# Optimization experiments

Measured on AMD Instinct MI355X. Metric: run time of the kernel, lower is better.

## Reference

```python
import jax, jax.numpy as jnp
import numpy as np

NUM_OBJECTS = 6          # self.NUM_OBJECTS
SCORE_THRESH = 1e-4      # self.score_tresh
NMS_THRESHS = jnp.asarray(np.arange(0.001, 1.0, 0.1), dtype=jnp.float32)  # 10 thresholds
K_CAND = 1024            # fixed-shape cap on (proposal,class) candidates per image
CLASS_OFFSET = 4096.0    # > max image coord; batched_nms per-class offset trick


def _iou_matrix(b):
    # b: [K,4] xyxy -> [K,K] IoU
    x1, y1, x2, y2 = b[:, 0], b[:, 1], b[:, 2], b[:, 3]
    area = (x2 - x1) * (y2 - y1)
    iw = jnp.clip(jnp.minimum(x2[:, None], x2[None, :]) - jnp.maximum(x1[:, None], x1[None, :]), 0.0)
    ih = jnp.clip(jnp.minimum(y2[:, None], y2[None, :]) - jnp.maximum(y1[:, None], y1[None, :]), 0.0)
    inter = iw * ih
    union = area[:, None] + area[None, :] - inter
    return jnp.where(union > 0, inter / union, 0.0)


def _greedy_nms(iou, valid, thresh):
    # candidates are pre-sorted by descending score; sequential greedy suppression
    K = valid.shape[0]
    ar = jnp.arange(K)
    def body(i, keep):
        sup = keep[i] & (iou[i] > thresh) & (ar > i)
        return keep & ~sup
    return jax.lax.fori_loop(0, K, body, valid)


def _per_image(logits, boxes, feats, hw):
    # logits [N,81], boxes [N,80,4], feats [N,2048], hw [2] (h,w)
    C = boxes.shape[1]
    probs = jax.nn.softmax(logits, axis=-1)[:, :C]          # drop background class
    h = hw[0].astype(boxes.dtype)
    w = hw[1].astype(boxes.dtype)
    b = jnp.stack([jnp.clip(boxes[..., 0], 0.0, w),         # clip to image
                   jnp.clip(boxes[..., 1], 0.0, h),
                   jnp.clip(boxes[..., 2], 0.0, w),
                   jnp.clip(boxes[..., 3], 0.0, h)], axis=-1)
    scores = probs.reshape(-1)                              # [N*C]
    vals, idx = jax.lax.top_k(jnp.where(scores > SCORE_THRESH, scores, -1.0), K_CAND)
    cand_valid = vals > SCORE_THRESH
    cb = b.reshape(-1, 4)[idx]                              # [K,4]
    cls = (idx % C).astype(boxes.dtype)
    prop = idx // C                                         # proposal row index
    iou = _iou_matrix(cb + cls[:, None] * CLASS_OFFSET)     # per-class NMS via offsets
    keeps = jax.vmap(lambda t: _greedy_nms(iou, cand_valid, t))(NMS_THRESHS)  # [T,K]
    counts = keeps.sum(axis=1)
    # torch loop: break at first (smallest) thresh yielding len(ids)==6, i.e. >=6 kept
    ok = counts >= NUM_OBJECTS
    t_sel = jnp.where(jnp.any(ok), jnp.argmax(ok), NMS_THRESHS.shape[0] - 1)
    keep = keeps[t_sel]
    _, top = jax.lax.top_k(jnp.where(keep, vals, -jnp.inf), NUM_OBJECTS)
    ids = prop[top]                                         # [6]
    return feats[ids].T                                     # [2048, 6] (permute(1,0))


def _forward(cls_logits, boxes, feature_pooled, image_hw):
    return jax.vmap(_per_image)(cls_logits, boxes, feature_pooled, image_hw)  # [B,2048,6]


def setup_inputs() -> dict:
    key = jax.random.key(0)
    k1, k2, k3, k4, k5 = jax.random.split(key, 5)
    B, N, C, D = 8, 1000, 80, 2048
    cls_logits = jax.random.normal(k1, (B, N, C + 1), dtype=jnp.float32)
    ctr = jax.random.uniform(k2, (B, N, C, 2), minval=0.0, maxval=800.0)
    sz = jax.random.uniform(k3, (B, N, C, 2), minval=8.0, maxval=200.0)
    boxes = jnp.concatenate([ctr - sz * 0.5, ctr + sz * 0.5], axis=-1).astype(jnp.float32)
    feature_pooled = jax.random.normal(k4, (B, N, D), dtype=jnp.float32)
    image_hw = jax.random.randint(k5, (B, 2), 600, 800, dtype=jnp.int32)
    return {"cls_logits": cls_logits, "boxes": boxes,
            "feature_pooled": feature_pooled, "image_hw": image_hw}


def reference(cls_logits, boxes, feature_pooled, image_hw):
    return _forward(cls_logits, boxes, feature_pooled, image_hw)
```

## Files before the change

### kernel.cpp

```cpp
#include <hip/hip_runtime.h>
#include <cmath>
#include <cstdint>

#define NB 8
#define NPROP 1000
#define NCLS 80
#define NLOG 81
#define KCAND 1024
#define NTH 10
#define DFEAT 2048
#define NOBJ 6
#define NSCORE (NPROP*NCLS)
#define HBLK 8
#define HCHUNK (NSCORE/HBLK)
#define PCHUNK (NPROP/HBLK)
#define CCAP 64
#define GMAX 2048

constexpr size_t OFF_SCORES = 0;
constexpr size_t OFF_H1     = OFF_SCORES + (size_t)NB * NSCORE * 4;
constexpr size_t OFF_H2     = OFF_H1 + (size_t)NB * HBLK * 2048 * 4;
constexpr size_t OFF_PIV    = OFF_H2 + (size_t)NB * HBLK * 2048 * 4;
constexpr size_t OFF_CBUF   = OFF_PIV + (size_t)NB * 8 * 4;
constexpr size_t OFF_GCNT   = OFF_CBUF + (size_t)NB * GMAX * 8;
constexpr size_t OFF_S1P    = OFF_GCNT + (size_t)NB * 4096 * 4;
constexpr size_t OFF_S2P    = OFF_S1P + (size_t)NB * 2048 * 4;
constexpr size_t OFF_CX1    = OFF_S2P + (size_t)NB * 2048 * 4;
constexpr size_t SZ_CARR    = (size_t)NB * KCAND * 4;
constexpr size_t OFF_CY1    = OFF_CX1 + SZ_CARR;
constexpr size_t OFF_CX2    = OFF_CY1 + SZ_CARR;
constexpr size_t OFF_CY2    = OFF_CX2 + SZ_CARR;
constexpr size_t OFF_CAREA  = OFF_CY2 + SZ_CARR;
constexpr size_t OFF_CPROP  = OFF_CAREA + SZ_CARR;
constexpr size_t OFF_VALIDW = OFF_CPROP + SZ_CARR;
constexpr size_t OFF_CCNT   = OFF_VALIDW + (size_t)NB * 16 * 8;
constexpr size_t OFF_CLIST  = OFF_CCNT + (size_t)NB * NCLS * 4;
constexpr size_t OFF_KEEPS  = OFF_CLIST + (size_t)NB * NCLS * CCAP * 4;

__device__ __forceinline__ float nms_th(int t) {
    return (float)(0.001 + 0.1 * (double)t);
}

__device__ __forceinline__ unsigned score_vkey(float v) {
    float vv = (v > 1e-4f) ? v : -1.0f;
    unsigned bits = __float_as_uint(vv);
    unsigned u = (bits & 0x80000000u) ? ~bits : (bits | 0x80000000u);
    return ~u;
}

__device__ __forceinline__ void scan2048(unsigned a, unsigned b, unsigned* pre,
                                         unsigned K, int* out_b, int* out_rem) {
    __shared__ unsigned wsum[16];
    int tid = threadIdx.x;
    unsigned p = a + b;
    unsigned x = p;
    #pragma unroll
    for (int d = 1; d < 64; d <<= 1) {
        unsigned y = __shfl_up(x, (unsigned)d, 64);
        if ((tid & 63) >= d) x += y;
    }
    if ((tid & 63) == 63) wsum[tid >> 6] = x;
    __syncthreads();
    if (tid < 16) {
        unsigned w = wsum[tid];
        #pragma unroll
        for (int d = 1; d < 16; d <<= 1) {
            unsigned y = __shfl_up(w, (unsigned)d, 64);
            if (tid >= d) w += y;
        }
        wsum[tid] = w;
    }
    __syncthreads();
    unsigned wex = (tid >= 64) ? wsum[(tid >> 6) - 1] : 0u;
    unsigned E = x + wex - p;
    pre[2 * tid]     = E;
    pre[2 * tid + 1] = E + a;
    if (E < K && E + a >= K)              { *out_b = 2 * tid;     *out_rem = (int)(K - E); }
    else if (E + a < K && E + a + b >= K) { *out_b = 2 * tid + 1; *out_rem = (int)(K - (E + a)); }
}

__global__ __launch_bounds__(1024) void k_softhist(const float* __restrict__ logits,
                                                   float* __restrict__ scores,
                                                   unsigned* __restrict__ hist1) {
    __shared__ unsigned hh[2048];
    int img = blockIdx.x >> 3, blk = blockIdx.x & 7;
    int tid = threadIdx.x, wid = tid >> 6, lane = tid & 63;
    hh[tid] = 0; hh[tid + 1024] = 0;
    __syncthreads();
    for (int p = wid; p < PCHUNK; p += 16) {
        int prop = blk * PCHUNK + p;
        const float* L = logits + ((size_t)img * NPROP + prop) * NLOG;
        float l0 = L[lane];
        float l1 = (lane < 17) ? L[64 + lane] : -INFINITY;
        float m = fmaxf(l0, l1);
        #pragma unroll
        for (int o = 32; o > 0; o >>= 1) m = fmaxf(m, __shfl_xor(m, o, 64));
        float e0 = expf(l0 - m);
        float e1 = (lane < 17) ? expf(l1 - m) : 0.f;
        float s = e0 + e1;
        #pragma unroll
        for (int o = 32; o > 0; o >>= 1) s += __shfl_xor(s, o, 64);
        float* op = scores + ((size_t)img * NPROP + prop) * NCLS;
        float p0 = e0 / s;
        op[lane] = p0;
        atomicAdd(&hh[score_vkey(p0) >> 21], 1u);
        if (lane < 16) {
            float p1 = e1 / s;
            op[64 + lane] = p1;
            atomicAdd(&hh[score_vkey(p1) >> 21], 1u);
        }
    }
    __syncthreads();
    unsigned* outp = hist1 + ((size_t)img * HBLK + blk) * 2048;
    outp[tid] = hh[tid];
    outp[tid + 1024] = hh[tid + 1024];
}

__global__ __launch_bounds__(1024) void k_hist2p(const float* __restrict__ scores,
                                                 const unsigned* __restrict__ hist1,
                                                 unsigned* __restrict__ hist2,
                                                 int* __restrict__ piv,
                                                 unsigned* __restrict__ gcg) {
    __shared__ unsigned hh[2048];
    __shared__ int sb, sr;
    int img = blockIdx.x >> 3, blk = blockIdx.x & 7;
    int tid = threadIdx.x;
    if (tid < 512) gcg[img * 4096 + blk * 512 + tid] = 0;
    if (tid == 0) { sb = 0; sr = 1; }
    __syncthreads();
    {
        unsigned a1 = 0, b1v = 0;
        const unsigned* h1 = hist1 + (size_t)img * HBLK * 2048;
        #pragma unroll
        for (int s = 0; s < HBLK; ++s) {
            a1  += h1[s * 2048 + 2 * tid];
            b1v += h1[s * 2048 + 2 * tid + 1];
        }
        scan2048(a1, b1v, hh, KCAND, &sb, &sr);
    }
    __syncthreads();
    hh[tid] = 0; hh[tid + 1024] = 0;
    __syncthreads();
    unsigned b1 = (unsigned)sb & 2047u;
    const float4* sc4 = (const float4*)(scores + (size_t)img * NSCORE + (size_t)blk * HCHUNK);
    #define H2S(val) { unsigned vk = score_vkey(val); \
                       if ((vk >> 21) == b1) atomicAdd(&hh[(vk >> 10) & 2047u], 1u); }
    for (int e4 = tid; e4 < HCHUNK / 4; e4 += 1024) {
        float4 v = sc4[e4];
        H2S(v.x) H2S(v.y) H2S(v.z) H2S(v.w)
    }
    #undef H2S
    __syncthreads();
    unsigned* outp = hist2 + ((size_t)img * HBLK + blk) * 2048;
    outp[tid] = hh[tid];
    outp[tid + 1024] = hh[tid + 1024];
    if (blk == 0 && tid == 0) {
        piv[img * 8 + 0] = sb;
        piv[img * 8 + 1] = sr;
    }
}

__global__ __launch_bounds__(1024) void k_gatherp(const float* __restrict__ scores,
                                                  const unsigned* __restrict__ hist1,
                                                  const unsigned* __restrict__ hist2,
                                                  int* __restrict__ piv,
                                                  unsigned long long* __restrict__ cbuf,
                                                  unsigned* __restrict__ gcg,
                                                  unsigned* __restrict__ s1pg,
                                                  unsigned* __restrict__ s2pg,
                                                  int* __restrict__ ccnt,
                                                  unsigned long long* __restrict__ validw,
                                                  unsigned long long* __restrict__ keeps) {
    __shared__ unsigned s1p[2048];
    __shared__ unsigned s2p[2048];
    __shared__ int sb1, sr1, sb2, sr2;
    int img = blockIdx.x >> 3, blk = blockIdx.x & 7;
    int tid = threadIdx.x;
    if (blockIdx.x == 0) {
        if (tid < NB * NCLS) ccnt[tid] = 0;
        if (tid >= 640 && tid < 640 + NB * 16) validw[tid - 640] = 0ULL;
    }
    if (blockIdx.x == 1) {
        for (int k = tid; k < NB * NTH * 16; k += 1024) keeps[k] = 0ULL;
    }
    if (tid == 0) { sb1 = 0; sr1 = 1; sb2 = 0; sr2 = 1; }
    __syncthreads();
    {
        unsigned a1 = 0, b1v = 0;
        const unsigned* h1 = hist1 + (size_t)img * HBLK * 2048;
        #pragma unroll
        for (int s = 0; s < HBLK; ++s) {
            a1  += h1[s * 2048 + 2 * tid];
            b1v += h1[s * 2048 + 2 * tid + 1];
        }
        scan2048(a1, b1v, s1p, KCAND, &sb1, &sr1);
    }
    __syncthreads();
    {
        unsigned a2 = 0, b2v = 0;
        const unsigned* h2 = hist2 + (size_t)img * HBLK * 2048;
        #pragma unroll
        for (int s = 0; s < HBLK; ++s) {
            a2  += h2[s * 2048 + 2 * tid];
            b2v += h2[s * 2048 + 2 * tid + 1];
        }
        scan2048(a2, b2v, s2p, (unsigned)sr1, &sb2, &sr2);
    }
    __syncthreads();
    unsigned b1 = (unsigned)sb1 & 2047u;
    unsigned sb2m = (unsigned)sb2 & 2047u;
    unsigned T22 = (b1 << 11) | sb2m;
    const float4* sc4 = (const float4*)(scores + (size_t)img * NSCORE + (size_t)blk * HCHUNK);
    unsigned long long* cb = cbuf + (size_t)img * GMAX;
    unsigned* gc = gcg + img * 4096;
    #define GAS(val, ei) { unsigned vk = score_vkey(val); unsigned t22 = vk >> 10; \
        if (t22 <= T22) { \
            unsigned h = vk >> 21; unsigned g, base; \
            if (h == b1) { unsigned sub = t22 & 2047u; g = 2048u + sub; base = s1p[b1] + s2p[sub]; } \
            else         { g = h;                      base = s1p[h]; } \
            unsigned slot = atomicAdd(&gc[g], 1u); \
            unsigned posn = base + slot; \
            if (posn < GMAX) cb[posn] = ((unsigned long long)vk << 32) | (unsigned)(ei); } }
    for (int e4 = tid; e4 < HCHUNK / 4; e4 += 1024) {
        float4 v = sc4[e4];
        int e = blk * HCHUNK + 4 * e4;
        GAS(v.x, e) GAS(v.y, e + 1) GAS(v.z, e + 2) GAS(v.w, e + 3)
    }
    #undef GAS
    if (blk == 0) {
        s1pg[img * 2048 + tid] = s1p[tid];
        s1pg[img * 2048 + tid + 1024] = s1p[tid + 1024];
        s2pg[img * 2048 + tid] = s2p[tid];
        s2pg[img * 2048 + tid + 1024] = s2p[tid + 1024];
        if (tid == 0) piv[img * 8 + 4] = sb2;
    }
}

__global__ __launch_bounds__(256) void k_rankcand(const unsigned long long* __restrict__ cbuf,
                                                  const int* __restrict__ piv,
                                                  const unsigned* __restrict__ gcg,
                                                  const unsigned* __restrict__ s1pg,
                                                  const unsigned* __restrict__ s2pg,
                                                  const float* __restrict__ boxes,
                                                  const int* __restrict__ hw,
                                                  float* __restrict__ cx1, float* __restrict__ cy1,
                                                  float* __restrict__ cx2, float* __restrict__ cy2,
                                                  float* __restrict__ car, int* __restrict__ cprop,
                                                  unsigned long long* __restrict__ validw,
                                                  int* __restrict__ ccnt, int* __restrict__ clist) {
    int img = blockIdx.x >> 3, sl = blockIdx.x & 7;
    int tid = threadIdx.x;
    unsigned b1   = (unsigned)piv[img * 8 + 0] & 2047u;
    unsigned sb2m = (unsigned)piv[img * 8 + 4] & 2047u;
    const unsigned* s1p = s1pg + img * 2048;
    const unsigned* s2p = s2pg + img * 2048;
    const unsigned* gc  = gcg + img * 4096;
    const unsigned long long* cb = cbuf + (size_t)img * GMAX;
    int cnt = (int)(s1p[b1] + s2p[sb2m] + gc[2048u + sb2m]);
    if (cnt > GMAX || cnt < 0) cnt = GMAX;
    int p = sl * 256 + tid;
    if (p < cnt) {
        unsigned long long akey = cb[p];
        unsigned vk = (unsigned)(akey >> 32);
        unsigned h = vk >> 21;
        unsigned base, gsz;
        if (h == b1) {
            unsigned sub = (vk >> 10) & 2047u;
            base = s1p[b1] + s2p[sub];
            gsz  = gc[2048u + sub];
        } else {
            base = s1p[h];
            gsz  = gc[h];
        }
        unsigned r_ = base;
        unsigned qe = base + gsz;
        if (qe > (unsigned)GMAX) qe = (unsigned)GMAX;
        for (unsigned q = base; q < qe; ++q)
            r_ += (cb[q] < akey) ? 1u : 0u;
        int r = (int)r_;
        unsigned idx = (unsigned)akey;
        int prop = (int)(idx / NCLS);
        if (r >= 0 && r < KCAND && (unsigned)prop < NPROP) {
            unsigned u = ~vk;
            const unsigned uth = __float_as_uint(1e-4f) | 0x80000000u;
            bool valid = u > uth;
            int cls = (int)(idx - (unsigned)prop * NCLS);
            const float4 bx = *(const float4*)(boxes + ((((size_t)img * NPROP + prop) * NCLS + cls) << 2));
            float fh = (float)hw[img * 2 + 0];
            float fw = (float)hw[img * 2 + 1];
            float x1 = fminf(fmaxf(bx.x, 0.f), fw);
            float y1 = fminf(fmaxf(bx.y, 0.f), fh);
            float x2 = fminf(fmaxf(bx.z, 0.f), fw);
            float y2 = fminf(fmaxf(bx.w, 0.f), fh);
            float offc = __fmul_rn((float)cls, 4096.0f);
            x1 = __fadd_rn(x1, offc); y1 = __fadd_rn(y1, offc);
            x2 = __fadd_rn(x2, offc); y2 = __fadd_rn(y2, offc);
            float area = __fmul_rn(__fsub_rn(x2, x1), __fsub_rn(y2, y1));
            int o = img * KCAND + r;
            cx1[o] = x1; cy1[o] = y1; cx2[o] = x2; cy2[o] = y2;
            car[o] = area; cprop[o] = prop;
            if (valid) atomicOr(&validw[img * 16 + (r >> 6)], 1ULL << (r & 63));
            int slot = atomicAdd(&ccnt[img * NCLS + cls], 1);
            if (slot < CCAP) clist[(img * NCLS + cls) * CCAP + slot] = r;
        }
    }
}

__global__ __launch_bounds__(256) void k_cnms(const int* __restrict__ ccnt,
                                              const int* __restrict__ clist,
                                              const float* __restrict__ cx1,
                                              const float* __restrict__ cy1,
                                              const float* __restrict__ cx2,
                                              const float* __restrict__ cy2,
                                              const float* __restrict__ car,
                                              const unsigned long long* __restrict__ validw,
                                              unsigned long long* __restrict__ keeps) {
    int gid  = blockIdx.x * 4 + (threadIdx.x >> 6);
    int lane = threadIdx.x & 63;
    if (gid >= NB * NCLS) return;
    int img = gid / NCLS, cls = gid - img * NCLS;
    int n = ccnt[img * NCLS + cls];
    if (n > CCAP) n = CCAP;
    if (n == 0) return;
    int r = (lane < n) ? clist[(img * NCLS + cls) * CCAP + lane] : 0x7fffffff;
    int pos = 0;
    for (int j = 0; j < n; ++j) {
        int rj = __shfl(r, j, 64);
        pos += (rj < r) ? 1 : 0;
    }
    int srt = 0;
    for (int j = 0; j < n; ++j) {
        int pj = __shfl(pos, j, 64);
        int rj = __shfl(r, j, 64);
        if (pj == lane) srt = rj;
    }
    srt &= (KCAND - 1);
    bool act = lane < n;
    int base = img * KCAND;
    float x1 = 0, y1 = 0, x2 = 0, y2 = 0, ar = 0;
    bool val = false;
    if (act) {
        x1 = cx1[base + srt]; y1 = cy1[base + srt];
        x2 = cx2[base + srt]; y2 = cy2[base + srt]; ar = car[base + srt];
        val = (validw[img * 16 + (srt >> 6)] >> (srt & 63)) & 1ULL;
    }
    unsigned long long m[NTH];
    #pragma unroll
    for (int t = 0; t < NTH; ++t) m[t] = 0ULL;
    for (int b = 0; b < n; ++b) {
        float xj1 = __shfl(x1, b, 64), yj1 = __shfl(y1, b, 64);
        float xj2 = __shfl(x2, b, 64), yj2 = __shfl(y2, b, 64);
        float aj  = __shfl(ar, b, 64);
        float iw = fmaxf(__fsub_rn(fminf(x2, xj2), fmaxf(x1, xj1)), 0.f);
        float ih = fmaxf(__fsub_rn(fminf(y2, yj2), fmaxf(y1, yj1)), 0.f);
        float inter = __fmul_rn(iw, ih);
        float uni   = __fsub_rn(__fadd_rn(ar, aj), inter);
        float iou   = (uni > 0.f) ? __fdiv_rn(inter, uni) : 0.f;
        if (act && b < lane) {
            #pragma unroll
            for (int t = 0; t < NTH; ++t)
                if (iou > nms_th(t)) m[t] |= 1ULL << b;
        }
    }
    unsigned long long vmask = __ballot(act && val);
    for (int t = 0; t < NTH; ++t) {
        unsigned long long keep = vmask;
        for (int it = 0; it <= n; ++it) {
            bool nk = act && val && ((m[t] & keep) == 0ULL);
            unsigned long long nb = __ballot(nk);
            if (nb == keep) break;
            keep = nb;
        }
        if (act && ((keep >> lane) & 1ULL))
            atomicOr(&keeps[((size_t)img * NTH + t) * 16 + (srt >> 6)], 1ULL << (srt & 63));
    }
}

__global__ __launch_bounds__(256) void k_selfeat(const unsigned long long* __restrict__ keeps,
                                                 const int* __restrict__ cprop,
                                                 const float* __restrict__ feats,
                                                 float* __restrict__ outp) {
    __shared__ int scnt[NTH];
    __shared__ unsigned long long skw[16];
    __shared__ int stsel;
    __shared__ int sids[NOBJ];
    int img = blockIdx.x >> 3;
    int tid = threadIdx.x;
    if (tid < NTH) scnt[tid] = 0;
    __syncthreads();
    if (tid < NTH * 16) {
        unsigned long long w = keeps[(size_t)img * NTH * 16 + tid];
        int pc = __popcll(w);
        if (pc) atomicAdd(&scnt[tid >> 4], pc);
    }
    __syncthreads();
    if (tid == 0) {
        int tsel = NTH - 1;
        for (int t = 0; t < NTH; ++t) if (scnt[t] >= NOBJ) { tsel = t; break; }
        stsel = tsel;
    }
    __syncthreads();
    if (tid < 16) skw[tid] = keeps[((size_t)img * NTH + stsel) * 16 + tid];
    __syncthreads();
    if (tid == 0) {
        int got = 0;
        for (int k = 0; k < 16 && got < NOBJ; ++k) {
            unsigned long long x = skw[k];
            while (x && got < NOBJ) {
                int b = __builtin_ctzll(x);
                int sid = cprop[img * KCAND + k * 64 + b];
                sids[got++] = ((unsigned)sid < NPROP) ? sid : 0;
                x &= x - 1;
            }
        }
        for (int k = 0; k < 16 && got < NOBJ; ++k) {
            unsigned long long x = ~skw[k];
            while (x && got < NOBJ) {
                int b = __builtin_ctzll(x);
                int sid = cprop[img * KCAND + k * 64 + b];
                sids[got++] = ((unsigned)sid < NPROP) ? sid : 0;
                x &= x - 1;
            }
        }
    }
    __syncthreads();
    int d = (blockIdx.x & 7) * 256 + tid;
    const float* fb = feats + (size_t)img * NPROP * DFEAT;
    float* ob = outp + ((size_t)img * DFEAT + d) * NOBJ;
    #pragma unroll
    for (int s = 0; s < NOBJ; ++s)
        ob[s] = fb[(size_t)sids[s] * DFEAT + d];
}

extern "C" void kernel_launch(void* const* d_in, const int* in_sizes, int n_in,
                              void* d_out, int out_size, void* d_ws, size_t ws_size,
                              hipStream_t stream) {
    const float* logits = (const float*)d_in[0];
    const float* boxes  = (const float*)d_in[1];
    const float* feats  = (const float*)d_in[2];
    const int*   hw     = (const int*)d_in[3];
    float* outp = (float*)d_out;

    char* ws = (char*)d_ws;
    float*              scores = (float*)(ws + OFF_SCORES);
    unsigned*           hist1  = (unsigned*)(ws + OFF_H1);
    unsigned*           hist2  = (unsigned*)(ws + OFF_H2);
    int*                piv    = (int*)(ws + OFF_PIV);
    unsigned long long* cbuf   = (unsigned long long*)(ws + OFF_CBUF);
    unsigned*           gcg    = (unsigned*)(ws + OFF_GCNT);
    unsigned*           s1pg   = (unsigned*)(ws + OFF_S1P);
    unsigned*           s2pg   = (unsigned*)(ws + OFF_S2P);
    float* cx1 = (float*)(ws + OFF_CX1);
    float* cy1 = (float*)(ws + OFF_CY1);
    float* cx2 = (float*)(ws + OFF_CX2);
    float* cy2 = (float*)(ws + OFF_CY2);
    float* car = (float*)(ws + OFF_CAREA);
    int*   cprop = (int*)(ws + OFF_CPROP);
    unsigned long long* validw = (unsigned long long*)(ws + OFF_VALIDW);
    int*   ccnt  = (int*)(ws + OFF_CCNT);
    int*   clist = (int*)(ws + OFF_CLIST);
    unsigned long long* keeps  = (unsigned long long*)(ws + OFF_KEEPS);

    k_softhist<<<NB * HBLK, 1024, 0, stream>>>(logits, scores, hist1);
    k_hist2p<<<NB * HBLK, 1024, 0, stream>>>(scores, hist1, hist2, piv, gcg);
    k_gatherp<<<NB * HBLK, 1024, 0, stream>>>(scores, hist1, hist2, piv, cbuf,
                                              gcg, s1pg, s2pg, ccnt, validw, keeps);
    k_rankcand<<<NB * HBLK, 256, 0, stream>>>(cbuf, piv, gcg, s1pg, s2pg, boxes, hw,
                                              cx1, cy1, cx2, cy2, car, cprop,
                                              validw, ccnt, clist);
    k_cnms<<<(NB * NCLS + 3) / 4, 256, 0, stream>>>(ccnt, clist, cx1, cy1, cx2, cy2,
                                                    car, validw, keeps);
    k_selfeat<<<NB * HBLK, 256, 0, stream>>>(keeps, cprop, feats, outp);
}
```

Measured before the change: 173.5 us.

## Fuse candidate ranking, per-class NMS and feature select into one per-image kernel

Replaces the rankcand, cnms and selfeat kernels with a single k_tail kernel, one 1024-thread block per image. It recomputes the histogram prefix scans locally and keeps candidate boxes, class lists, valid and keep masks in shared memory instead of global scratch. This removes two kernel launches, the global round trips and the zero-initialisation writes. The cost is that each image now runs on a single block, so the tail stages have only 8 blocks of parallelism and the feature gather is done by one block per image.

Result: slower. 212.1 us (+22.2%).

```diff
diff --git a/kernel.cpp b/kernel.cpp
--- a/kernel.cpp
+++ b/kernel.cpp
@@ -20,22 +20,8 @@
 constexpr size_t OFF_SCORES = 0;
 constexpr size_t OFF_H1     = OFF_SCORES + (size_t)NB * NSCORE * 4;
 constexpr size_t OFF_H2     = OFF_H1 + (size_t)NB * HBLK * 2048 * 4;
-constexpr size_t OFF_PIV    = OFF_H2 + (size_t)NB * HBLK * 2048 * 4;
-constexpr size_t OFF_CBUF   = OFF_PIV + (size_t)NB * 8 * 4;
+constexpr size_t OFF_CBUF   = OFF_H2 + (size_t)NB * HBLK * 2048 * 4;
 constexpr size_t OFF_GCNT   = OFF_CBUF + (size_t)NB * GMAX * 8;
-constexpr size_t OFF_S1P    = OFF_GCNT + (size_t)NB * 4096 * 4;
-constexpr size_t OFF_S2P    = OFF_S1P + (size_t)NB * 2048 * 4;
-constexpr size_t OFF_CX1    = OFF_S2P + (size_t)NB * 2048 * 4;
-constexpr size_t SZ_CARR    = (size_t)NB * KCAND * 4;
-constexpr size_t OFF_CY1    = OFF_CX1 + SZ_CARR;
-constexpr size_t OFF_CX2    = OFF_CY1 + SZ_CARR;
-constexpr size_t OFF_CY2    = OFF_CX2 + SZ_CARR;
-constexpr size_t OFF_CAREA  = OFF_CY2 + SZ_CARR;
-constexpr size_t OFF_CPROP  = OFF_CAREA + SZ_CARR;
-constexpr size_t OFF_VALIDW = OFF_CPROP + SZ_CARR;
-constexpr size_t OFF_CCNT   = OFF_VALIDW + (size_t)NB * 16 * 8;
-constexpr size_t OFF_CLIST  = OFF_CCNT + (size_t)NB * NCLS * 4;
-constexpr size_t OFF_KEEPS  = OFF_CLIST + (size_t)NB * NCLS * CCAP * 4;
 
 __device__ __forceinline__ float nms_th(int t) {
     return (float)(0.001 + 0.1 * (double)t);
@@ -119,7 +105,6 @@
 __global__ __launch_bounds__(1024) void k_hist2p(const float* __restrict__ scores,
                                                  const unsigned* __restrict__ hist1,
                                                  unsigned* __restrict__ hist2,
-                                                 int* __restrict__ piv,
                                                  unsigned* __restrict__ gcg) {
     __shared__ unsigned hh[2048];
     __shared__ int sb, sr;
@@ -154,35 +139,18 @@
     unsigned* outp = hist2 + ((size_t)img * HBLK + blk) * 2048;
     outp[tid] = hh[tid];
     outp[tid + 1024] = hh[tid + 1024];
-    if (blk == 0 && tid == 0) {
-        piv[img * 8 + 0] = sb;
-        piv[img * 8 + 1] = sr;
-    }
 }
 
 __global__ __launch_bounds__(1024) void k_gatherp(const float* __restrict__ scores,
                                                   const unsigned* __restrict__ hist1,
                                                   const unsigned* __restrict__ hist2,
-                                                  int* __restrict__ piv,
                                                   unsigned long long* __restrict__ cbuf,
-                                                  unsigned* __restrict__ gcg,
-                                                  unsigned* __restrict__ s1pg,
-                                                  unsigned* __restrict__ s2pg,
-                                                  int* __restrict__ ccnt,
-                                                  unsigned long long* __restrict__ validw,
-                                                  unsigned long long* __restrict__ keeps) {
+                                                  unsigned* __restrict__ gcg) {
     __shared__ unsigned s1p[2048];
     __shared__ unsigned s2p[2048];
     __shared__ int sb1, sr1, sb2, sr2;
     int img = blockIdx.x >> 3, blk = blockIdx.x & 7;
     int tid = threadIdx.x;
-    if (blockIdx.x == 0) {
-        if (tid < NB * NCLS) ccnt[tid] = 0;
-        if (tid >= 640 && tid < 640 + NB * 16) validw[tid - 640] = 0ULL;
-    }
-    if (blockIdx.x == 1) {
-        for (int k = tid; k < NB * NTH * 16; k += 1024) keeps[k] = 0ULL;
-    }
     if (tid == 0) { sb1 = 0; sr1 = 1; sb2 = 0; sr2 = 1; }
     __syncthreads();
     {
@@ -227,180 +195,191 @@
         GAS(v.x, e) GAS(v.y, e + 1) GAS(v.z, e + 2) GAS(v.w, e + 3)
     }
     #undef GAS
-    if (blk == 0) {
-        s1pg[img * 2048 + tid] = s1p[tid];
-        s1pg[img * 2048 + tid + 1024] = s1p[tid + 1024];
-        s2pg[img * 2048 + tid] = s2p[tid];
-        s2pg[img * 2048 + tid + 1024] = s2p[tid + 1024];
-        if (tid == 0) piv[img * 8 + 4] = sb2;
-    }
-}
-
-__global__ __launch_bounds__(256) void k_rankcand(const unsigned long long* __restrict__ cbuf,
-                                                  const int* __restrict__ piv,
-                                                  const unsigned* __restrict__ gcg,
-                                                  const unsigned* __restrict__ s1pg,
-                                                  const unsigned* __restrict__ s2pg,
-                                                  const float* __restrict__ boxes,
-                                                  const int* __restrict__ hw,
-                                                  float* __restrict__ cx1, float* __restrict__ cy1,
-                                                  float* __restrict__ cx2, float* __restrict__ cy2,
-                                                  float* __restrict__ car, int* __restrict__ cprop,
-                                                  unsigned long long* __restrict__ validw,
-                                                  int* __restrict__ ccnt, int* __restrict__ clist) {
-    int img = blockIdx.x >> 3, sl = blockIdx.x & 7;
+}
+
+__global__ __launch_bounds__(1024) void k_tail(const unsigned long long* __restrict__ cbuf,
+                                               const unsigned* __restrict__ gcg,
+                                               const unsigned* __restrict__ hist1,
+                                               const unsigned* __restrict__ hist2,
+                                               const float* __restrict__ boxes,
+                                               const int* __restrict__ hw,
+                                               const float* __restrict__ feats,
+                                               float* __restrict__ outp) {
+    __shared__ unsigned s1p[2048];
+    __shared__ unsigned s2p[2048];
+    __shared__ float scx1[KCAND], scy1[KCAND], scx2[KCAND], scy2[KCAND], scar[KCAND];
+    __shared__ int   scprop[KCAND];
+    __shared__ int   sclist[NCLS * CCAP];
+    __shared__ int   sccnt[NCLS];
+    __shared__ unsigned long long svalid[16];
+    __shared__ unsigned long long skeeps[NTH * 16];
+    __shared__ int sb1, sr1, sb2, sr2, stsel;
+    __shared__ int scnt6[NTH];
+    __shared__ unsigned long long skw[16];
+    __shared__ int sids[NOBJ];
+
+    int img = blockIdx.x;
     int tid = threadIdx.x;
-    unsigned b1   = (unsigned)piv[img * 8 + 0] & 2047u;
-    unsigned sb2m = (unsigned)piv[img * 8 + 4] & 2047u;
-    const unsigned* s1p = s1pg + img * 2048;
-    const unsigned* s2p = s2pg + img * 2048;
-    const unsigned* gc  = gcg + img * 4096;
-    const unsigned long long* cb = cbuf + (size_t)img * GMAX;
-    int cnt = (int)(s1p[b1] + s2p[sb2m] + gc[2048u + sb2m]);
-    if (cnt > GMAX || cnt < 0) cnt = GMAX;
-    int p = sl * 256 + tid;
-    if (p < cnt) {
-        unsigned long long akey = cb[p];
-        unsigned vk = (unsigned)(akey >> 32);
-        unsigned h = vk >> 21;
-        unsigned base, gsz;
-        if (h == b1) {
-            unsigned sub = (vk >> 10) & 2047u;
-            base = s1p[b1] + s2p[sub];
-            gsz  = gc[2048u + sub];
-        } else {
-            base = s1p[h];
-            gsz  = gc[h];
-        }
-        unsigned r_ = base;
-        unsigned qe = base + gsz;
-        if (qe > (unsigned)GMAX) qe = (unsigned)GMAX;
-        for (unsigned q = base; q < qe; ++q)
-            r_ += (cb[q] < akey) ? 1u : 0u;
-        int r = (int)r_;
-        unsigned idx = (unsigned)akey;
-        int prop = (int)(idx / NCLS);
-        if (r >= 0 && r < KCAND && (unsigned)prop < NPROP) {
-            unsigned u = ~vk;
-            const unsigned uth = __float_as_uint(1e-4f) | 0x80000000u;
-            bool valid = u > uth;
-            int cls = (int)(idx - (unsigned)prop * NCLS);
-            const float4 bx = *(const float4*)(boxes + ((((size_t)img * NPROP + prop) * NCLS + cls) << 2));
-            float fh = (float)hw[img * 2 + 0];
-            float fw = (float)hw[img * 2 + 1];
-            float x1 = fminf(fmaxf(bx.x, 0.f), fw);
-            float y1 = fminf(fmaxf(bx.y, 0.f), fh);
-            float x2 = fminf(fmaxf(bx.z, 0.f), fw);
-            float y2 = fminf(fmaxf(bx.w, 0.f), fh);
-            float offc = __fmul_rn((float)cls, 4096.0f);
-            x1 = __fadd_rn(x1, offc); y1 = __fadd_rn(y1, offc);
-            x2 = __fadd_rn(x2, offc); y2 = __fadd_rn(y2, offc);
-            float area = __fmul_rn(__fsub_rn(x2, x1), __fsub_rn(y2, y1));
-            int o = img * KCAND + r;
-            cx1[o] = x1; cy1[o] = y1; cx2[o] = x2; cy2[o] = y2;
-            car[o] = area; cprop[o] = prop;
-            if (valid) atomicOr(&validw[img * 16 + (r >> 6)], 1ULL << (r & 63));
-            int slot = atomicAdd(&ccnt[img * NCLS + cls], 1);
-            if (slot < CCAP) clist[(img * NCLS + cls) * CCAP + slot] = r;
-        }
-    }
-}
-
-__global__ __launch_bounds__(256) void k_cnms(const int* __restrict__ ccnt,
-                                              const int* __restrict__ clist,
-                                              const float* __restrict__ cx1,
-                                              const float* __restrict__ cy1,
-                                              const float* __restrict__ cx2,
-                                              const float* __restrict__ cy2,
-                                              const float* __restrict__ car,
-                                              const unsigned long long* __restrict__ validw,
-                                              unsigned long long* __restrict__ keeps) {
-    int gid  = blockIdx.x * 4 + (threadIdx.x >> 6);
-    int lane = threadIdx.x & 63;
-    if (gid >= NB * NCLS) return;
-    int img = gid / NCLS, cls = gid - img * NCLS;
-    int n = ccnt[img * NCLS + cls];
-    if (n > CCAP) n = CCAP;
-    if (n == 0) return;
-    int r = (lane < n) ? clist[(img * NCLS + cls) * CCAP + lane] : 0x7fffffff;
-    int pos = 0;
-    for (int j = 0; j < n; ++j) {
-        int rj = __shfl(r, j, 64);
-        pos += (rj < r) ? 1 : 0;
-    }
-    int srt = 0;
-    for (int j = 0; j < n; ++j) {
-        int pj = __shfl(pos, j, 64);
-        int rj = __shfl(r, j, 64);
-        if (pj == lane) srt = rj;
-    }
-    srt &= (KCAND - 1);
-    bool act = lane < n;
-    int base = img * KCAND;
-    float x1 = 0, y1 = 0, x2 = 0, y2 = 0, ar = 0;
-    bool val = false;
-    if (act) {
-        x1 = cx1[base + srt]; y1 = cy1[base + srt];
-        x2 = cx2[base + srt]; y2 = cy2[base + srt]; ar = car[base + srt];
-        val = (validw[img * 16 + (srt >> 6)] >> (srt & 63)) & 1ULL;
-    }
-    unsigned long long m[NTH];
-    #pragma unroll
-    for (int t = 0; t < NTH; ++t) m[t] = 0ULL;
-    for (int b = 0; b < n; ++b) {
-        float xj1 = __shfl(x1, b, 64), yj1 = __shfl(y1, b, 64);
-        float xj2 = __shfl(x2, b, 64), yj2 = __shfl(y2, b, 64);
-        float aj  = __shfl(ar, b, 64);
-        float iw = fmaxf(__fsub_rn(fminf(x2, xj2), fmaxf(x1, xj1)), 0.f);
-        float ih = fmaxf(__fsub_rn(fminf(y2, yj2), fmaxf(y1, yj1)), 0.f);
-        float inter = __fmul_rn(iw, ih);
-        float uni   = __fsub_rn(__fadd_rn(ar, aj), inter);
-        float iou   = (uni > 0.f) ? __fdiv_rn(inter, uni) : 0.f;
-        if (act && b < lane) {
+
+    scprop[tid] = 0;
+    if (tid < NCLS) sccnt[tid] = 0;
+    if (tid < 16) svalid[tid] = 0ULL;
+    if (tid < NTH * 16) skeeps[tid] = 0ULL;
+    if (tid < NTH) scnt6[tid] = 0;
+    if (tid == 0) { sb1 = 0; sr1 = 1; sb2 = 0; sr2 = 1; }
+    __syncthreads();
+
+    {
+        unsigned a1 = 0, b1v = 0;
+        const unsigned* h1 = hist1 + (size_t)img * HBLK * 2048;
+        #pragma unroll
+        for (int s = 0; s < HBLK; ++s) {
+            a1  += h1[s * 2048 + 2 * tid];
+            b1v += h1[s * 2048 + 2 * tid + 1];
+        }
+        scan2048(a1, b1v, s1p, KCAND, &sb1, &sr1);
+    }
+    __syncthreads();
+    {
+        unsigned a2 = 0, b2v = 0;
+        const unsigned* h2 = hist2 + (size_t)img * HBLK * 2048;
+        #pragma unroll
+        for (int s = 0; s < HBLK; ++s) {
+            a2  += h2[s * 2048 + 2 * tid];
+            b2v += h2[s * 2048 + 2 * tid + 1];
+        }
+        scan2048(a2, b2v, s2p, (unsigned)sr1, &sb2, &sr2);
+    }
+    __syncthreads();
+
+    {
+        unsigned b1 = (unsigned)sb1 & 2047u;
+        unsigned sb2m = (unsigned)sb2 & 2047u;
+        const unsigned* gc = gcg + img * 4096;
+        const unsigned long long* cb = cbuf + (size_t)img * GMAX;
+        int cnt = (int)(s1p[b1] + s2p[sb2m] + gc[2048u + sb2m]);
+        if (cnt > GMAX || cnt < 0) cnt = GMAX;
+        for (int p = tid; p < cnt; p += 1024) {
+            unsigned long long akey = cb[p];
+            unsigned vk = (unsigned)(akey >> 32);
+            unsigned h = vk >> 21;
+            unsigned base, gsz;
+            if (h == b1) {
+                unsigned sub = (vk >> 10) & 2047u;
+                base = s1p[b1] + s2p[sub];
+                gsz  = gc[2048u + sub];
+            } else {
+                base = s1p[h];
+                gsz  = gc[h];
+            }
+            unsigned r_ = base;
+            unsigned qe = base + gsz;
+            if (qe > (unsigned)GMAX) qe = (unsigned)GMAX;
+            for (unsigned q = base; q < qe; ++q)
+                r_ += (cb[q] < akey) ? 1u : 0u;
+            int r = (int)r_;
+            unsigned idx = (unsigned)akey;
+            int prop = (int)(idx / NCLS);
+            if (r >= 0 && r < KCAND && (unsigned)prop < NPROP) {
+                unsigned u = ~vk;
+                const unsigned uth = __float_as_uint(1e-4f) | 0x80000000u;
+                bool valid = u > uth;
+                int cls = (int)(idx - (unsigned)prop * NCLS);
+                const float4 bx = *(const float4*)(boxes + ((((size_t)img * NPROP + prop) * NCLS + cls) << 2));
+                float fh = (float)hw[img * 2 + 0];
+                float fw = (float)hw[img * 2 + 1];
+                float x1 = fminf(fmaxf(bx.x, 0.f), fw);
+                float y1 = fminf(fmaxf(bx.y, 0.f), fh);
+                float x2 = fminf(fmaxf(bx.z, 0.f), fw);
+                float y2 = fminf(fmaxf(bx.w, 0.f), fh);
+                float offc = __fmul_rn((float)cls, 4096.0f);
+                x1 = __fadd_rn(x1, offc); y1 = __fadd_rn(y1, offc);
+                x2 = __fadd_rn(x2, offc); y2 = __fadd_rn(y2, offc);
+                float area = __fmul_rn(__fsub_rn(x2, x1), __fsub_rn(y2, y1));
+                scx1[r] = x1; scy1[r] = y1; scx2[r] = x2; scy2[r] = y2;
+                scar[r] = area; scprop[r] = prop;
+                if (valid) atomicOr(&svalid[r >> 6], 1ULL << (r & 63));
+                int slot = atomicAdd(&sccnt[cls], 1);
+                if (slot < CCAP) sclist[cls * CCAP + slot] = r;
+            }
+        }
+    }
+    __syncthreads();
+
+    {
+        int wv = tid >> 6, lane = tid & 63;
+        for (int cls = wv; cls < NCLS; cls += 16) {
+            int n = sccnt[cls];
+            if (n > CCAP) n = CCAP;
+            if (n == 0) continue;
+            int rk = (lane < n) ? sclist[cls * CCAP + lane] : 0x7fffffff;
+            int pos = 0;
+            for (int j = 0; j < n; ++j) {
+                int rj = __shfl(rk, j, 64);
+                pos += (rj < rk) ? 1 : 0;
+            }
+            int srt = 0;
+            for (int j = 0; j < n; ++j) {
+                int pj = __shfl(pos, j, 64);
+                int rj = __shfl(rk, j, 64);
+                if (pj == lane) srt = rj;
+            }
+            srt &= (KCAND - 1);
+            bool act = lane < n;
+            float x1 = 0, y1 = 0, x2 = 0, y2 = 0, ar = 0;
+            bool val = false;
+            if (act) {
+                x1 = scx1[srt]; y1 = scy1[srt];
+                x2 = scx2[srt]; y2 = scy2[srt]; ar = scar[srt];
+                val = (svalid[srt >> 6] >> (srt & 63)) & 1ULL;
+            }
+            unsigned long long m[NTH];
             #pragma unroll
-            for (int t = 0; t < NTH; ++t)
-                if (iou > nms_th(t)) m[t] |= 1ULL << b;
-        }
-    }
-    unsigned long long vmask = __ballot(act && val);
-    for (int t = 0; t < NTH; ++t) {
-        unsigned long long keep = vmask;
-        for (int it = 0; it <= n; ++it) {
-            bool nk = act && val && ((m[t] & keep) == 0ULL);
-            unsigned long long nb = __ballot(nk);
-            if (nb == keep) break;
-            keep = nb;
-        }
-        if (act && ((keep >> lane) & 1ULL))
-            atomicOr(&keeps[((size_t)img * NTH + t) * 16 + (srt >> 6)], 1ULL << (srt & 63));
-    }
-}
-
-__global__ __launch_bounds__(256) void k_selfeat(const unsigned long long* __restrict__ keeps,
-                                                 const int* __restrict__ cprop,
-                                                 const float* __restrict__ feats,
-                                                 float* __restrict__ outp) {
-    __shared__ int scnt[NTH];
-    __shared__ unsigned long long skw[16];
-    __shared__ int stsel;
-    __shared__ int sids[NOBJ];
-    int img = blockIdx.x >> 3;
-    int tid = threadIdx.x;
-    if (tid < NTH) scnt[tid] = 0;
-    __syncthreads();
+            for (int t = 0; t < NTH; ++t) m[t] = 0ULL;
+            for (int b = 0; b < n; ++b) {
+                float xj1 = __shfl(x1, b, 64), yj1 = __shfl(y1, b, 64);
+                float xj2 = __shfl(x2, b, 64), yj2 = __shfl(y2, b, 64);
+                float aj  = __shfl(ar, b, 64);
+                float iw = fmaxf(__fsub_rn(fminf(x2, xj2), fmaxf(x1, xj1)), 0.f);
+                float ih = fmaxf(__fsub_rn(fminf(y2, yj2), fmaxf(y1, yj1)), 0.f);
+                float inter = __fmul_rn(iw, ih);
+                float uni   = __fsub_rn(__fadd_rn(ar, aj), inter);
+                float iou   = (uni > 0.f) ? __fdiv_rn(inter, uni) : 0.f;
+                if (act && b < lane) {
+                    #pragma unroll
+                    for (int t = 0; t < NTH; ++t)
+                        if (iou > nms_th(t)) m[t] |= 1ULL << b;
+                }
+            }
+            unsigned long long vmask = __ballot(act && val);
+            for (int t = 0; t < NTH; ++t) {
+                unsigned long long keep = vmask;
+                for (int it = 0; it <= n; ++it) {
+                    bool nk = act && val && ((m[t] & keep) == 0ULL);
+                    unsigned long long nb = __ballot(nk);
+                    if (nb == keep) break;
+                    keep = nb;
+                }
+                if (act && ((keep >> lane) & 1ULL))
+                    atomicOr(&skeeps[t * 16 + (srt >> 6)], 1ULL << (srt & 63));
+            }
+        }
+    }
+    __syncthreads();
+
     if (tid < NTH * 16) {
-        unsigned long long w = keeps[(size_t)img * NTH * 16 + tid];
+        unsigned long long w = skeeps[tid];
         int pc = __popcll(w);
-        if (pc) atomicAdd(&scnt[tid >> 4], pc);
+        if (pc) atomicAdd(&scnt6[tid >> 4], pc);
     }
     __syncthreads();
     if (tid == 0) {
         int tsel = NTH - 1;
-        for (int t = 0; t < NTH; ++t) if (scnt[t] >= NOBJ) { tsel = t; break; }
+        for (int t = 0; t < NTH; ++t) if (scnt6[t] >= NOBJ) { tsel = t; break; }
         stsel = tsel;
     }
     __syncthreads();
-    if (tid < 16) skw[tid] = keeps[((size_t)img * NTH + stsel) * 16 + tid];
+    if (tid < 16) skw[tid] = skeeps[stsel * 16 + tid];
     __syncthreads();
     if (tid == 0) {
         int got = 0;
@@ -408,7 +387,7 @@
             unsigned long long x = skw[k];
             while (x && got < NOBJ) {
                 int b = __builtin_ctzll(x);
-                int sid = cprop[img * KCAND + k * 64 + b];
+                int sid = scprop[k * 64 + b];
                 sids[got++] = ((unsigned)sid < NPROP) ? sid : 0;
                 x &= x - 1;
             }
@@ -417,19 +396,21 @@
             unsigned long long x = ~skw[k];
             while (x && got < NOBJ) {
                 int b = __builtin_ctzll(x);
-                int sid = cprop[img * KCAND + k * 64 + b];
+                int sid = scprop[k * 64 + b];
                 sids[got++] = ((unsigned)sid < NPROP) ? sid : 0;
                 x &= x - 1;
             }
         }
     }
     __syncthreads();
-    int d = (blockIdx.x & 7) * 256 + tid;
+
     const float* fb = feats + (size_t)img * NPROP * DFEAT;
-    float* ob = outp + ((size_t)img * DFEAT + d) * NOBJ;
-    #pragma unroll
-    for (int s = 0; s < NOBJ; ++s)
-        ob[s] = fb[(size_t)sids[s] * DFEAT + d];
+    for (int d = tid; d < DFEAT; d += 1024) {
+        float* ob = outp + ((size_t)img * DFEAT + d) * NOBJ;
+        #pragma unroll
+        for (int s = 0; s < NOBJ; ++s)
+            ob[s] = fb[(size_t)sids[s] * DFEAT + d];
+    }
 }
 
 extern "C" void kernel_launch(void* const* d_in, const int* in_sizes, int n_in,
@@ -445,30 +426,11 @@
     float*              scores = (float*)(ws + OFF_SCORES);
     unsigned*           hist1  = (unsigned*)(ws + OFF_H1);
     unsigned*           hist2  = (unsigned*)(ws + OFF_H2);
-    int*                piv    = (int*)(ws + OFF_PIV);
     unsigned long long* cbuf   = (unsigned long long*)(ws + OFF_CBUF);
     unsigned*           gcg    = (unsigned*)(ws + OFF_GCNT);
-    unsigned*           s1pg   = (unsigned*)(ws + OFF_S1P);
-    unsigned*           s2pg   = (unsigned*)(ws + OFF_S2P);
-    float* cx1 = (float*)(ws + OFF_CX1);
-    float* cy1 = (float*)(ws + OFF_CY1);
-    float* cx2 = (float*)(ws + OFF_CX2);
-    float* cy2 = (float*)(ws + OFF_CY2);
-    float* car = (float*)(ws + OFF_CAREA);
-    int*   cprop = (int*)(ws + OFF_CPROP);
-    unsigned long long* validw = (unsigned long long*)(ws + OFF_VALIDW);
-    int*   ccnt  = (int*)(ws + OFF_CCNT);
-    int*   clist = (int*)(ws + OFF_CLIST);
-    unsigned long long* keeps  = (unsigned long long*)(ws + OFF_KEEPS);
 
     k_softhist<<<NB * HBLK, 1024, 0, stream>>>(logits, scores, hist1);
-    k_hist2p<<<NB * HBLK, 1024, 0, stream>>>(scores, hist1, hist2, piv, gcg);
-    k_gatherp<<<NB * HBLK, 1024, 0, stream>>>(scores, hist1, hist2, piv, cbuf,
-                                              gcg, s1pg, s2pg, ccnt, validw, keeps);
-    k_rankcand<<<NB * HBLK, 256, 0, stream>>>(cbuf, piv, gcg, s1pg, s2pg, boxes, hw,
-                                              cx1, cy1, cx2, cy2, car, cprop,
-                                              validw, ccnt, clist);
-    k_cnms<<<(NB * NCLS + 3) / 4, 256, 0, stream>>>(ccnt, clist, cx1, cy1, cx2, cy2,
-                                                    car, validw, keeps);
-    k_selfeat<<<NB * HBLK, 256, 0, stream>>>(keeps, cprop, feats, outp);
-}
+    k_hist2p<<<NB * HBLK, 1024, 0, stream>>>(scores, hist1, hist2, gcg);
+    k_gatherp<<<NB * HBLK, 1024, 0, stream>>>(scores, hist1, hist2, cbuf, gcg);
+    k_tail<<<NB, 1024, 0, stream>>>(cbuf, gcg, hist1, hist2, boxes, hw, feats, outp);
+}
```
